# Kernel optimization log

Measured on AMD Instinct MI355X. Metric: run time of the kernel, lower is better.

## Reference

```python
import jax, jax.numpy as jnp
import numpy as np

N = 128  # image size
J = 4    # number of scales
L = 4    # number of orientations


def make_morlet_filters(n, j_max, n_angles):
    """Fixed Morlet filter bank in Fourier space, shape [J, L, N, N] (real)."""
    freqs = np.fft.fftfreq(n) * 2.0 * np.pi
    kx = freqs[:, None] * np.ones((1, n))
    ky = np.ones((n, 1)) * freqs[None, :]
    filters = np.zeros((j_max, n_angles, n, n), dtype=np.float32)
    for j in range(j_max):
        k0 = 3.0 * np.pi / 4.0 / (2.0 ** j)   # central frequency of scale j
        sigma = 0.8 * (2.0 ** j)               # gaussian width in space
        for l in range(n_angles):
            theta = np.pi * l / n_angles
            k0x, k0y = k0 * np.cos(theta), k0 * np.sin(theta)
            beta = np.exp(-0.5 * sigma ** 2 * k0 ** 2)  # zero-mean correction
            g_shift = np.exp(-0.5 * sigma ** 2 * ((kx - k0x) ** 2 + (ky - k0y) ** 2))
            g_zero = np.exp(-0.5 * sigma ** 2 * (kx ** 2 + ky ** 2))
            filters[j, l] = g_shift - beta * g_zero
    return jnp.asarray(filters)


PSI = make_morlet_filters(N, J, L)  # fixed (non-learned) filter bank
VALID_PAIRS = [(j1, j2) for j1 in range(J) for j2 in range(J) if j2 > j1]  # 6 pairs


def setup_inputs() -> dict:
    key = jax.random.key(0)
    k1, k2, k3, k4, k5 = jax.random.split(key, 5)
    B = 64
    return {
        "image_batch": jax.random.normal(k1, (B, N, N), dtype=jnp.float32),
        "fc1_w": jax.random.normal(k2, (4, 11), dtype=jnp.float32) * 0.3,
        "fc1_b": jax.random.normal(k3, (4,), dtype=jnp.float32) * 0.1,
        "fc2_w": jax.random.normal(k4, (10, 4), dtype=jnp.float32) * 0.3,
        "fc2_b": jax.random.normal(k5, (10,), dtype=jnp.float32) * 0.1,
    }


def _scattering(image):
    # image: [B, N, N]
    i_hat = jnp.fft.fft2(image)  # [B,N,N] complex64
    s0 = jnp.mean(image, axis=(1, 2))  # [B]
    # first order: |x * psi_{j1,l1}|  -> [B,J,L,N,N]
    u1 = jnp.abs(jnp.fft.ifft2(i_hat[:, None, None] * PSI[None]))
    s1 = jnp.mean(u1, axis=(2, 3, 4))  # [B,J] averaged over orientations+space
    u1_hat = jnp.fft.fft2(u1)  # [B,J,L,N,N]
    # second order: only j2 > j1 (others NaN in original and masked out)
    s2_list = []
    for (j1, j2) in VALID_PAIRS:
        # [B, L1, L2, N, N]
        field = jnp.fft.ifft2(u1_hat[:, j1, :, None] * PSI[j2][None, None])
        s2_list.append(jnp.mean(jnp.abs(field), axis=(1, 2, 3, 4)))
    s2 = jnp.stack(s2_list, axis=1)  # [B,6]
    return jnp.concatenate([s0[:, None], s1, s2], axis=1)  # [B,11]


def reference(image_batch, fc1_w, fc1_b, fc2_w, fc2_b):
    coeffs = _scattering(image_batch)                      # [B,11]
    h = jax.nn.relu(coeffs @ fc1_w.T + fc1_b)              # [B,4]
    return jax.nn.sigmoid(h @ fc2_w.T + fc2_b)             # [B,10]
```

## Files before the change

kernel.cpp:

```cpp
#include <hip/hip_runtime.h>
#include <math.h>

#define NN   128
#define SS   129
#define TT   512
#define NPIX 16384
#define EPT  32
#define SG   65
#define SG32 33


__device__ __forceinline__ float2 cmul(float2 a, float2 w) {
    return make_float2(a.x * w.x - a.y * w.y, a.x * w.y + a.y * w.x);
}
__device__ __forceinline__ float2 cmulc(float2 a, float2 w) {
    return make_float2(a.x * w.x + a.y * w.y, a.y * w.x - a.x * w.y);
}

template<int SGN>
__device__ __forceinline__ void fft4(float2* f) {
    float2 t0 = make_float2(f[0].x + f[2].x, f[0].y + f[2].y);
    float2 t1 = make_float2(f[0].x - f[2].x, f[0].y - f[2].y);
    float2 t2 = make_float2(f[1].x + f[3].x, f[1].y + f[3].y);
    float2 t3 = make_float2(f[1].x - f[3].x, f[1].y - f[3].y);
// ... 73 lines not shown
    if (tid < 128) {
        float s, c;
        __sincosf((float)tid * 0.04908738521234052f, &s, &c);
        tw[tid] = make_float2(c, s);
    }
}

__device__ __forceinline__ float pass32x4(float4* __restrict__ P4a,
                                          float4* __restrict__ P4b,
                                          const float2* __restrict__ tw, int tid) {
    __syncthreads();
    {
        float4* P = (tid & 256) ? P4b : P4a;
        int line = tid & 31, a = (tid >> 5) & 7;
        float2 f0[4], f1[4];
        #pragma unroll
        for (int kb = 0; kb < 4; ++kb) {
            float4 v = P[(4 * a + kb) * SG32 + line];
            f0[kb] = make_float2(v.x, v.y); f1[kb] = make_float2(v.z, v.w);
        }
        fft4<1>(f0); fft4<1>(f1);
        #pragma unroll
        for (int t = 0; t < 4; ++t) {
            float2 w = tw[4 * t * a];
            float2 aa = cmul(f0[t], w), d = cmul(f1[t], w);
            P[(4 * a + t) * SG32 + line] = make_float4(aa.x, aa.y, d.x, d.y);
        }
    }
    __syncthreads();
    if (tid < 256) {
        float4* P = (tid & 128) ? P4b : P4a;
        int line = tid & 31, t = (tid >> 5) & 3;
        float2 f0[8], f1[8];
        #pragma unroll
        for (int a = 0; a < 8; ++a) {
            float4 v = P[(4 * a + t) * SG32 + line];
            f0[a] = make_float2(v.x, v.y); f1[a] = make_float2(v.z, v.w);
        }
        fft8<1>(f0); fft8<1>(f1);
        #pragma unroll
        for (int n1 = 0; n1 < 8; ++n1)
            P[(4 * n1 + t) * SG32 + line] =
                make_float4(f0[n1].x, f0[n1].y, f1[n1].x, f1[n1].y);
    }
    __syncthreads();
    {
        float4* P = (tid & 256) ? P4b : P4a;
        int row = tid & 31, a = (tid >> 5) & 7;
        float4* R = P + row * SG32 + 4 * a;
        float2 f0[4], f1[4];
        #pragma unroll
        for (int kb = 0; kb < 4; ++kb) {
            float4 v = R[kb];
            f0[kb] = make_float2(v.x, v.y); f1[kb] = make_float2(v.z, v.w);
        }
        fft4<1>(f0); fft4<1>(f1);
        #pragma unroll
        for (int t = 0; t < 4; ++t) {
            float2 w = tw[4 * t * a];
            float2 aa = cmul(f0[t], w), d = cmul(f1[t], w);
            R[t] = make_float4(aa.x, aa.y, d.x, d.y);
        }
    }
    __syncthreads();
    float a2 = 0.f;
    if (tid < 256) {
        float4* P = (tid & 128) ? P4b : P4a;
        int row = tid & 31, t = (tid >> 5) & 3;
        float4* R = P + row * SG32 + t;
        float2 f0[8], f1[8];
        #pragma unroll
        for (int a = 0; a < 8; ++a) {
            float4 v = R[4 * a];
            f0[a] = make_float2(v.x, v.y); f1[a] = make_float2(v.z, v.w);
        }
        fft8<1>(f0); fft8<1>(f1);
        #pragma unroll
        for (int n1 = 0; n1 < 8; ++n1) {
            a2 += sqrtf(f0[n1].x * f0[n1].x + f0[n1].y * f0[n1].y);
            a2 += sqrtf(f1[n1].x * f1[n1].x + f1[n1].y * f1[n1].y);
        }
    }
    return a2;
}

template<int ES, int LS>
__device__ __forceinline__ void fwdA(float2* __restrict__ F,
                                     const float2* __restrict__ tw, int tid) {
    #pragma unroll
    for (int i = 0; i < 4; ++i) {
        int u = i * TT + tid;
        int t = u >> 7, x = u & 127;
        float2* M = F + x * LS;
        float2 f[8];
        #pragma unroll
        for (int n1 = 0; n1 < 8; ++n1) f[n1] = M[(t + 16 * n1) * ES];
        fft8<-1>(f);
        #pragma unroll
        for (int ka = 0; ka < 8; ++ka)
            M[(t + 16 * ka) * ES] = cmulc(f[ka], tw[t * ka]);
    }
}

template<int ES, int LS>
__device__ __forceinline__ void fwdB(float2* __restrict__ F, int tid) {
    #pragma unroll
    for (int i = 0; i < 2; ++i) {
        int u = i * TT + tid;
        int ka = u >> 7, x = u & 127;
        float2* M = F + x * LS;
        float2 g[16];
        #pragma unroll
        for (int t = 0; t < 16; ++t) g[t] = M[(16 * ka + t) * ES];
        fft16<-1>(g);
        #pragma unroll
        for (int kb = 0; kb < 16; ++kb) M[(16 * ka + kb) * ES] = g[kb];
    }
}

__device__ __forceinline__ void fwdB_col_capture(const float2* __restrict__ F, int tid,
                                                 float2* __restrict__ uh) {
    #pragma unroll
    for (int i = 0; i < 2; ++i) {
        int u = i * TT + tid;
        int ka = u >> 7, c = u & 127;
        float2 g[16];
        #pragma unroll
        for (int t = 0; t < 16; ++t) g[t] = F[(16 * ka + t) * SS + c];
        fft16<-1>(g);
        #pragma unroll
        for (int kb = 0; kb < 16; ++kb) uh[i * 16 + kb] = g[kb];
    }
}

template<int ES, int LS>
__device__ __forceinline__ void invA(float2* __restrict__ F,
                                     const float2* __restrict__ tw, int tid) {
    #pragma unroll
    for (int i = 0; i < 2; ++i) {
        int u = i * TT + tid;
        int ka = u >> 7, x = u & 127;
        float2* M = F + x * LS;
        float2 g[16];
        #pragma unroll
        for (int kb = 0; kb < 16; ++kb) g[kb] = M[(16 * ka + kb) * ES];
        fft16<1>(g);
        #pragma unroll
        for (int t = 0; t < 16; ++t)
            M[(16 * ka + t) * ES] = cmul(g[t], tw[t * ka]);
    }
}

template<int ES, int LS>
__device__ __forceinline__ void invB(float2* __restrict__ F, int tid) {
    #pragma unroll
    for (int i = 0; i < 4; ++i) {
        int u = i * TT + tid;
        int t = u >> 7, x = u & 127;
        float2* M = F + x * LS;
        float2 f[8];
        #pragma unroll
        for (int ka = 0; ka < 8; ++ka) f[ka] = M[(16 * ka + t) * ES];
        fft8<1>(f);
        #pragma unroll
        for (int nh = 0; nh < 8; ++nh) M[(t + 16 * nh) * ES] = f[nh];
    }
// ... 25 lines not shown
}

__global__ __attribute__((amdgpu_flat_work_group_size(TT, TT), amdgpu_waves_per_eu(2, 2)))
void k_pre(const float* __restrict__ img,
           float* __restrict__ psi,
           float2* __restrict__ ihat,
           float* __restrict__ coeffs) {
    __shared__ float2 F[NN * SS];
    __shared__ float2 tw[128];
    __shared__ float red[TT / 64];
    int blk = blockIdx.x, tid = threadIdx.x;
    if (blk >= 64) {
        if (blk == 80) {
            for (int i = tid; i < 64 * 11; i += TT)
                if (i % 11 != 0) coeffs[i] = 0.f;
            return;
        }
        int f = blk - 64;
        int j = f >> 2, l = f & 3;
        float k0    = 2.35619449019234493f / (float)(1 << j);
        float sigma = 0.8f * (float)(1 << j);
        float s2    = sigma * sigma;
        float theta = 0.78539816339744831f * (float)l;
        float k0x = k0 * cosf(theta);
        float k0y = k0 * sinf(theta);
        float beta = expf(-0.5f * s2 * k0 * k0);
        const float FSTEP = 0.04908738521234052f;
        float* dst = psi + (size_t)f * NPIX;
        for (int i = tid; i < NPIX; i += TT) {
            int pr = i >> 7, pc = i & 127;
            int kr = (pr >> 4) + 8 * (pr & 15);
            int kc = (pc >> 4) + 8 * (pc & 15);
            float fr = (float)(kr < 64 ? kr : kr - 128) * FSTEP;
            float fc = (float)(kc < 64 ? kc : kc - 128) * FSTEP;
            float dx = fr - k0x, dy = fc - k0y;
            float g1 = expf(-0.5f * s2 * (dx * dx + dy * dy));
            float g0 = expf(-0.5f * s2 * (fr * fr + fc * fc));
            dst[i] = g1 - beta * g0;
        }
        return;
    }
    int b = blk;
    buildTw(tw, tid);
    const float* im = img + (size_t)b * NPIX;
    float acc = 0.f;
    #pragma unroll
    for (int k = 0; k < EPT; ++k) {
        int e = k * TT + tid;
        float v = im[e];
        acc += v;
        F[(e >> 7) * SS + (e & 127)] = make_float2(v, 0.f);
    }
    float ws = waveReduceSum(acc);
    if ((tid & 63) == 0) red[tid >> 6] = ws;
    __syncthreads();
    if (tid == 0) {
        float t = 0.f;
        #pragma unroll
        for (int w = 0; w < TT / 64; ++w) t += red[w];
        coeffs[b * 11 + 0] = t * (1.f / 16384.f);
    }
    fwdA<1, SS>(F, tw, tid);  __syncthreads();
    fwdB<1, SS>(F, tid);      __syncthreads();
    fwdA<SS, 1>(F, tw, tid);  __syncthreads();
    float2 uh[32];
    fwdB_col_capture(F, tid, uh);
    float2* dst = ihat + (size_t)b * NPIX;
    #pragma unroll
    for (int i = 0; i < 2; ++i) {
        int u = i * TT + tid;
        int ka = u >> 7, c = u & 127;
        #pragma unroll
        for (int kb = 0; kb < 16; ++kb)
            dst[(16 * ka + kb) * NN + c] = uh[i * 16 + kb];
    }
}

__global__ __attribute__((amdgpu_flat_work_group_size(TT, TT), amdgpu_waves_per_eu(2, 2)))
void k_scat_big(const float2* __restrict__ ihat,
                const float* __restrict__ psi,
                float* __restrict__ coeffs) {
    __shared__ __align__(16) float2 F[16640];
    __shared__ float2 tw[128];
    float4* G4a = (float4*)F;
    float4* G4b = (float4*)(F + 8320);
    float2* G2a = F;
    float2* G2b = F + 4160;
    float2* G2c = F + 8320;
    float2* G2d = F + 12480;
    float4* P4a = (float4*)F;
    float4* P4b = (float4*)F + 1056;
    int tid = threadIdx.x;
    int x = blockIdx.x;
    int b = x & 63, l1 = x >> 6;
    const float2* ih = ihat + (size_t)b * NPIX;
    const float*  p1 = psi + (size_t)l1 * NPIX;
    buildTw(tw, tid);

    const float S1_128 = 9.3132257461547852e-10f;
    const float S2TR   = 5.6843418860808015e-14f;
    const float S2_03  = 2.2737367544323206e-13f;

    int kalo = tid >> 7, c = tid & 127;
    {
        #pragma unroll
        for (int i = 0; i < 2; ++i) {
            int ka = kalo + 4 * i;
            float2 g[16];
            #pragma unroll
            for (int kb = 0; kb < 16; ++kb) {
                int e = (16 * ka + kb) * NN + c;
                float2 z = ih[e];
                float  p = p1[e];
                g[kb] = make_float2(z.x * p, z.y * p);
            }
            fft16<1>(g);
            #pragma unroll
            for (int t = 0; t < 16; ++t)
                F[(16 * ka + t) * SS + c] = cmul(g[t], tw[t * ka]);
        }
    }
    __syncthreads();
    invB<SS, 1>(F, tid);      __syncthreads();
    invA<1, SS>(F, tw, tid);  __syncthreads();
    float acc = 0.f;
    invBmag_fwdA_row(F, tw, tid, acc);
    float ws1 = waveReduceSum(acc);
    if ((tid & 63) == 0) atomicAdd(&coeffs[b * 11 + 1], ws1 * S1_128);
    __syncthreads();
    fwdB<1, SS>(F, tid);      __syncthreads();
    fwdA<SS, 1>(F, tw, tid);  __syncthreads();
    float2 uh[32];
    fwdB_col_capture(F, tid, uh);
    __syncthreads();

    int m = c & 15;
    bool colKeep = (m < 4) || (m >= 12);
    int pc64 = 8 * (c >> 4) + ((m < 4) ? m : (m - 8));

    {
        const int ORW[4] = {21, 15, 0, -15};
        const int OCW[4] = { 0, 15, 21,  15};
        int fc = (c >> 4) + 8 * (c & 15);
        bool ckw[4]; int pcw[4];
        #pragma unroll
        for (int w = 0; w < 4; ++w) {
            int dc = (fc - OCW[w]) & 127;
            ckw[w] = (dc < 32) || (dc >= 96);
            int uc = (dc < 32) ? dc : (dc - 64);
            pcw[w] = 8 * (uc & 7) + (uc >> 3);
        }
        #pragma unroll
        for (int i = 0; i < 2; ++i) {
            int ka = kalo + 4 * i;
            #pragma unroll
            for (int kb = 0; kb < 16; ++kb) {
                int fr = ka + 8 * kb;
                float2 z = uh[i * 16 + kb];
                int e = (16 * ka + kb) * NN + c;
                #pragma unroll
                for (int w = 0; w < 4; ++w) {
                    if (ckw[w]) {
                        int dr = (fr - ORW[w]) & 127;
                        if (dr < 32 || dr >= 96) {
                            int ur = (dr < 32) ? dr : (dr - 64);
                            int pr = 8 * (ur & 7) + (ur >> 3);
                            float pv = psi[(size_t)(4 + w) * NPIX + e];
                            float2* G = (w == 0) ? G2a : (w == 1) ? G2b
                                       : (w == 2) ? G2c : G2d;
                            G[pr * SG + pcw[w]] = make_float2(z.x * pv, z.y * pv);
                        }
                    }
                }
            }
        }
        __syncthreads();
        {
            int col = tid & 63, k8 = tid >> 6;
            float2 f0[8], f1[8], f2[8], f3[8];
            #pragma unroll
            for (int kb = 0; kb < 8; ++kb) {
                int o = (8 * k8 + kb) * SG + col;
                f0[kb] = G2a[o]; f1[kb] = G2b[o]; f2[kb] = G2c[o]; f3[kb] = G2d[o];
            }
            fft8<1>(f0); fft8<1>(f1); fft8<1>(f2); fft8<1>(f3);
            #pragma unroll
            for (int q = 0; q < 8; ++q) {
                float2 w = tw[2 * q * k8];
                int o = (8 * k8 + q) * SG + col;
                G2a[o] = cmul(f0[q], w); G2b[o] = cmul(f1[q], w);
                G2c[o] = cmul(f2[q], w); G2d[o] = cmul(f3[q], w);
            }
        }
        __syncthreads();
        {
            int col = tid & 63, q = tid >> 6;
            float2 f0[8], f1[8], f2[8], f3[8];
            #pragma unroll
            for (int k8 = 0; k8 < 8; ++k8) {
                int o = (8 * k8 + q) * SG + col;
                f0[k8] = G2a[o]; f1[k8] = G2b[o]; f2[k8] = G2c[o]; f3[k8] = G2d[o];
            }
            fft8<1>(f0); fft8<1>(f1); fft8<1>(f2); fft8<1>(f3);
            #pragma unroll
            for (int n1 = 0; n1 < 8; ++n1) {
                int o = (8 * n1 + q) * SG + col;
                G2a[o] = f0[n1]; G2b[o] = f1[n1]; G2c[o] = f2[n1]; G2d[o] = f3[n1];
            }
        }
        __syncthreads();
        {
            int row = tid & 63, k8 = tid >> 6;
            int base = row * SG + 8 * k8;
            float2 f0[8], f1[8], f2[8], f3[8];
            #pragma unroll
            for (int kb = 0; kb < 8; ++kb) {
                f0[kb] = G2a[base + kb]; f1[kb] = G2b[base + kb];
                f2[kb] = G2c[base + kb]; f3[kb] = G2d[base + kb];
            }
            fft8<1>(f0); fft8<1>(f1); fft8<1>(f2); fft8<1>(f3);
            #pragma unroll
            for (int q = 0; q < 8; ++q) {
                float2 w = tw[2 * q * k8];
                G2a[base + q] = cmul(f0[q], w); G2b[base + q] = cmul(f1[q], w);
                G2c[base + q] = cmul(f2[q], w); G2d[base + q] = cmul(f3[q], w);
            }
        }
        __syncthreads();
        float a2 = 0.f;
        {
            int row = tid & 63, q = tid >> 6;
            int base = row * SG + q;
            float2 f0[8], f1[8], f2[8], f3[8];
            #pragma unroll
            for (int k8 = 0; k8 < 8; ++k8) {
                int o = base + 8 * k8;
                f0[k8] = G2a[o]; f1[k8] = G2b[o]; f2[k8] = G2c[o]; f3[k8] = G2d[o];
            }
            fft8<1>(f0); fft8<1>(f1); fft8<1>(f2); fft8<1>(f3);
            #pragma unroll
            for (int n1 = 0; n1 < 8; ++n1) {
                a2 += sqrtf(f0[n1].x * f0[n1].x + f0[n1].y * f0[n1].y);
                a2 += sqrtf(f1[n1].x * f1[n1].x + f1[n1].y * f1[n1].y);
                a2 += sqrtf(f2[n1].x * f2[n1].x + f2[n1].y * f2[n1].y);
                a2 += sqrtf(f3[n1].x * f3[n1].x + f3[n1].y * f3[n1].y);
            }
        }
        float ws2 = waveReduceSum(a2);
        if ((tid & 63) == 0) atomicAdd(&coeffs[b * 11 + 5 + 0], ws2 * S2TR);
        __syncthreads();
    }

    {
        const float* p0 = psi + (size_t)8 * NPIX;
        const float* pq1 = p0 + NPIX;
        const float* pq2 = pq1 + NPIX;
        const float* pq3 = pq2 + NPIX;
        if (colKeep) {
            #pragma unroll
            for (int i = 0; i < 2; ++i) {
                int ka = kalo + 4 * i;
                #pragma unroll
                for (int kb = 0; kb < 16; ++kb) {
                    if (kb < 4 || kb >= 12) {
                        int pr64 = 8 * ka + ((kb < 4) ? kb : (kb - 8));
                        float2 z = uh[i * 16 + kb];
                        int e = (16 * ka + kb) * NN + c;
                        float a0 = p0[e], a1 = pq1[e], a2f = pq2[e], a3 = pq3[e];
                        G4a[pr64 * SG + pc64] =
                            make_float4(z.x * a0, z.y * a0, z.x * a1, z.y * a1);
                        G4b[pr64 * SG + pc64] =
                            make_float4(z.x * a2f, z.y * a2f, z.x * a3, z.y * a3);
                    }
                }
            }
        }
        __syncthreads();
        {
            int col = tid & 63, k8 = tid >> 6;
            float2 f0[8], f1[8], f2[8], f3[8];
            #pragma unroll
            for (int kb = 0; kb < 8; ++kb) {
                int o = (8 * k8 + kb) * SG + col;
                float4 v = G4a[o];
                f0[kb] = make_float2(v.x, v.y); f1[kb] = make_float2(v.z, v.w);
                float4 u = G4b[o];
                f2[kb] = make_float2(u.x, u.y); f3[kb] = make_float2(u.z, u.w);
            }
            fft8<1>(f0); fft8<1>(f1); fft8<1>(f2); fft8<1>(f3);
            #pragma unroll
            for (int q = 0; q < 8; ++q) {
                float2 w = tw[2 * q * k8];
                int o = (8 * k8 + q) * SG + col;
                float2 a = cmul(f0[q], w), d = cmul(f1[q], w);
                G4a[o] = make_float4(a.x, a.y, d.x, d.y);
                float2 a2c = cmul(f2[q], w), d2 = cmul(f3[q], w);
                G4b[o] = make_float4(a2c.x, a2c.y, d2.x, d2.y);
            }
        }
        __syncthreads();
        {
            int col = tid & 63, q = tid >> 6;
            float2 f0[8], f1[8], f2[8], f3[8];
            #pragma unroll
            for (int k8 = 0; k8 < 8; ++k8) {
                int o = (8 * k8 + q) * SG + col;
                float4 v = G4a[o];
                f0[k8] = make_float2(v.x, v.y); f1[k8] = make_float2(v.z, v.w);
                float4 u = G4b[o];
                f2[k8] = make_float2(u.x, u.y); f3[k8] = make_float2(u.z, u.w);
            }
            fft8<1>(f0); fft8<1>(f1); fft8<1>(f2); fft8<1>(f3);
            #pragma unroll
            for (int n1 = 0; n1 < 8; ++n1) {
                int o = (8 * n1 + q) * SG + col;
                G4a[o] = make_float4(f0[n1].x, f0[n1].y, f1[n1].x, f1[n1].y);
                G4b[o] = make_float4(f2[n1].x, f2[n1].y, f3[n1].x, f3[n1].y);
            }
        }
        __syncthreads();
        {
            int row = tid & 63, k8 = tid >> 6;
            int base = row * SG + 8 * k8;
            float2 f0[8], f1[8], f2[8], f3[8];
            #pragma unroll
            for (int kb = 0; kb < 8; ++kb) {
                float4 v = G4a[base + kb];
                f0[kb] = make_float2(v.x, v.y); f1[kb] = make_float2(v.z, v.w);
                float4 u = G4b[base + kb];
                f2[kb] = make_float2(u.x, u.y); f3[kb] = make_float2(u.z, u.w);
            }
            fft8<1>(f0); fft8<1>(f1); fft8<1>(f2); fft8<1>(f3);
            #pragma unroll
            for (int q = 0; q < 8; ++q) {
                float2 w = tw[2 * q * k8];
                float2 a = cmul(f0[q], w), d = cmul(f1[q], w);
                G4a[base + q] = make_float4(a.x, a.y, d.x, d.y);
                float2 a2c = cmul(f2[q], w), d2 = cmul(f3[q], w);
                G4b[base + q] = make_float4(a2c.x, a2c.y, d2.x, d2.y);
            }
        }
        __syncthreads();
        float a2 = 0.f;
        {
            int row = tid & 63, q = tid >> 6;
            int base = row * SG + q;
            float2 f0[8], f1[8], f2[8], f3[8];
            #pragma unroll
            for (int k8 = 0; k8 < 8; ++k8) {
                float4 v = G4a[base + 8 * k8];
                f0[k8] = make_float2(v.x, v.y); f1[k8] = make_float2(v.z, v.w);
                float4 u = G4b[base + 8 * k8];
                f2[k8] = make_float2(u.x, u.y); f3[k8] = make_float2(u.z, u.w);
            }
            fft8<1>(f0); fft8<1>(f1); fft8<1>(f2); fft8<1>(f3);
            #pragma unroll
            for (int n1 = 0; n1 < 8; ++n1) {
                a2 += sqrtf(f0[n1].x * f0[n1].x + f0[n1].y * f0[n1].y);
                a2 += sqrtf(f1[n1].x * f1[n1].x + f1[n1].y * f1[n1].y);
                a2 += sqrtf(f2[n1].x * f2[n1].x + f2[n1].y * f2[n1].y);
                a2 += sqrtf(f3[n1].x * f3[n1].x + f3[n1].y * f3[n1].y);
            }
        }
        float ws2 = waveReduceSum(a2);
        if ((tid & 63) == 0) atomicAdd(&coeffs[b * 11 + 5 + 1], ws2 * S2TR);
        __syncthreads();
    }

    {
        bool ck32 = (m < 2) || (m >= 14);
        int pc32 = 4 * (c >> 4) + ((m < 2) ? m : (m - 12));
        const float* p0 = psi + (size_t)12 * NPIX;
        const float* pq1 = p0 + NPIX;
        const float* pq2 = pq1 + NPIX;
        const float* pq3 = pq2 + NPIX;
        if (ck32) {
            #pragma unroll
            for (int i = 0; i < 2; ++i) {
                int ka = kalo + 4 * i;
                #pragma unroll
                for (int kb = 0; kb < 16; ++kb) {
                    if (kb < 2 || kb >= 14) {
                        int pr32 = 4 * ka + ((kb < 2) ? kb : (kb - 12));
                        float2 z = uh[i * 16 + kb];
                        int e = (16 * ka + kb) * NN + c;
                        float a0 = p0[e], a1 = pq1[e], a2f = pq2[e], a3 = pq3[e];
                        P4a[pr32 * SG32 + pc32] =
                            make_float4(z.x * a0, z.y * a0, z.x * a1, z.y * a1);
                        P4b[pr32 * SG32 + pc32] =
                            make_float4(z.x * a2f, z.y * a2f, z.x * a3, z.y * a3);
                    }
                }
            }
        }
        float a2 = pass32x4(P4a, P4b, tw, tid);
        float ws2 = waveReduceSum(a2);
        if ((tid & 63) == 0) atomicAdd(&coeffs[b * 11 + 5 + 2], ws2 * S2_03);
    }
}

__global__ __attribute__((amdgpu_flat_work_group_size(TT, TT), amdgpu_waves_per_eu(4, 4)))
void k_scat_small(const float2* __restrict__ ihat,
                  const float* __restrict__ psi,
                  float* __restrict__ coeffs) {
    __shared__ __align__(16) float2 S[8320];
    __shared__ float2 tw[128];
    float2* G2  = S;
    float2* G32 = S;
    float4* G4  = (float4*)S;
    float4* P4a = (float4*)S;
    float4* P4b = (float4*)S + 1056;
    float2* H32 = S + 6144;
    int tid = threadIdx.x;
    int x = blockIdx.x;
    int b = x & 63, l1 = (x >> 6) & 3;
    int t0 = x >> 8;
    int j1 = (t0 == 0) ? 1 : (t0 + 1);
    const float2* ih = ihat + (size_t)b * NPIX;
    const float*  p1 = psi + (size_t)(j1 * 4 + l1) * NPIX;
    buildTw(tw, tid);

    const float S1_64 = 3.7252902984619141e-9f;
    const float S1_32 = 1.4901161193847656e-8f;
    const float S2_32 = 9.0949470177292824e-13f;
    const float S2_V  = 2.2737367544323206e-13f;

    int kalo = tid >> 7, c = tid & 127;

    if (t0 == 0) {
        const int OR1[4] = {21, 15, 0, -15};
        const int OC1[4] = { 0, 15, 21,  15};
        int fc = (c >> 4) + 8 * (c & 15);
        int dc = (fc - OC1[l1]) & 127;
        bool ck = (dc < 32) || (dc >= 96);
        int ucw = (dc < 32) ? dc : (dc - 64);
        int pcd = 8 * (ucw & 7) + (ucw >> 3);
        if (ck) {
            #pragma unroll
            for (int i = 0; i < 2; ++i) {
                int ka = kalo + 4 * i;
                #pragma unroll
                for (int kb = 0; kb < 16; ++kb) {
                    int fr = ka + 8 * kb;
                    int dr = (fr - OR1[l1]) & 127;
                    if (dr < 32 || dr >= 96) {
                        int ur = (dr < 32) ? dr : (dr - 64);
                        int pr = 8 * (ur & 7) + (ur >> 3);
                        int e = (16 * ka + kb) * NN + c;
                        float2 z = ih[e];
                        float  p = p1[e];
                        G2[pr * SG + pcd] = make_float2(z.x * p, z.y * p);
                    }
                }
            }
        }
        __syncthreads();
        {
            int col = tid & 63, k8 = tid >> 6;
            float2 f[8];
            #pragma unroll
            for (int kb = 0; kb < 8; ++kb) f[kb] = G2[(8 * k8 + kb) * SG + col];
            fft8<1>(f);
            #pragma unroll
            for (int q = 0; q < 8; ++q)
                G2[(8 * k8 + q) * SG + col] = cmul(f[q], tw[2 * q * k8]);
        }
        __syncthreads();
        {
            int col = tid & 63, q = tid >> 6;
            float2 f[8];
            #pragma unroll
            for (int k8 = 0; k8 < 8; ++k8) f[k8] = G2[(8 * k8 + q) * SG + col];
            fft8<1>(f);
            #pragma unroll
            for (int n1 = 0; n1 < 8; ++n1) G2[(8 * n1 + q) * SG + col] = f[n1];
        }
        __syncthreads();
        {
            int row = tid & 63, k8 = tid >> 6;
            float2* R = G2 + row * SG + 8 * k8;
            float2 f[8];
            #pragma unroll
            for (int kb = 0; kb < 8; ++kb) f[kb] = R[kb];
            fft8<1>(f);
            #pragma unroll
            for (int q = 0; q < 8; ++q) R[q] = cmul(f[q], tw[2 * q * k8]);
        }
        __syncthreads();
        float acc = 0.f;
        {
            int row = tid & 63, q = tid >> 6;
            float2* R = G2 + row * SG + q;
            float2 f[8];
            #pragma unroll
            for (int k8 = 0; k8 < 8; ++k8) f[k8] = R[8 * k8];
            fft8<1>(f);
            #pragma unroll
            for (int n1 = 0; n1 < 8; ++n1) {
                float mg = sqrtf(f[n1].x * f[n1].x + f[n1].y * f[n1].y);
                acc += mg;
                f[n1] = make_float2(mg, 0.f);
            }
            fft8<-1>(f);
            #pragma unroll
            for (int ka = 0; ka < 8; ++ka)
                R[8 * ka] = cmulc(f[ka], tw[2 * q * ka]);
        }
        float ws1 = waveReduceSum(acc);
        if ((tid & 63) == 0) atomicAdd(&coeffs[b * 11 + 2], ws1 * S1_64);
        __syncthreads();
        {
            int row2 = tid & 63, ka = tid >> 6;
            float2* R2 = G2 + row2 * SG + 8 * ka;
            float2 g[8];
            #pragma unroll
            for (int t = 0; t < 8; ++t) g[t] = R2[t];
            fft8<-1>(g);
            #pragma unroll
            for (int kb = 0; kb < 8; ++kb) R2[kb] = g[kb];
        }
        __syncthreads();
        {
            int col = tid & 63, t = tid >> 6;
            float2 g[8];
            #pragma unroll
            for (int n1 = 0; n1 < 8; ++n1) g[n1] = G2[(t + 8 * n1) * SG + col];
            fft8<-1>(g);
            #pragma unroll
            for (int ka = 0; ka < 8; ++ka)
                G2[(t + 8 * ka) * SG + col] = cmulc(g[ka], tw[2 * t * ka]);
        }
        __syncthreads();
        float2 vh[8];
        int c6 = tid & 63, ka8 = tid >> 6;
        {
            float2 g[8];
            #pragma unroll
            for (int t = 0; t < 8; ++t) g[t] = G2[(8 * ka8 + t) * SG + c6];
            fft8<-1>(g);
            #pragma unroll
            for (int kb = 0; kb < 8; ++kb) vh[kb] = g[kb];
        }
        __syncthreads();

        int uc64 = 8 * (c6 & 7) + (c6 >> 3);
        int fc128 = (uc64 < 32) ? uc64 : (uc64 + 64);
        int scI = 16 * (fc128 & 7) + (fc128 >> 3);
        int se[8];
        #pragma unroll
        for (int kb = 0; kb < 8; ++kb) {
            int ur = 8 * kb + ka8;
            int fr128 = (ur < 32) ? ur : (ur + 64);
            se[kb] = (16 * (fr128 & 7) + (fr128 >> 3)) * NN + scI;
        }

        {
            for (int half = 0; half < 2; ++half) {
                const float* p2a = psi + (size_t)(8 + 2 * half) * NPIX;
                const float* p2b = p2a + NPIX;
                #pragma unroll
                for (int kb = 0; kb < 8; ++kb) {
                    float pa = p2a[se[kb]], pb = p2b[se[kb]];
                    G4[(8 * ka8 + kb) * SG + c6] =
                        make_float4(vh[kb].x * pa, vh[kb].y * pa,
                                    vh[kb].x * pb, vh[kb].y * pb);
                }
                __syncthreads();
                {
                    int col = tid & 63, k8 = tid >> 6;
                    float2 f0[8], f1[8];
                    #pragma unroll
                    for (int kb = 0; kb < 8; ++kb) {
                        float4 v = G4[(8 * k8 + kb) * SG + col];
                        f0[kb] = make_float2(v.x, v.y); f1[kb] = make_float2(v.z, v.w);
                    }
                    fft8<1>(f0); fft8<1>(f1);
                    #pragma unroll
                    for (int q = 0; q < 8; ++q) {
                        float2 w = tw[2 * q * k8];
                        float2 a = cmul(f0[q], w), d = cmul(f1[q], w);
                        G4[(8 * k8 + q) * SG + col] = make_float4(a.x, a.y, d.x, d.y);
                    }
                }
                __syncthreads();
                {
                    int col = tid & 63, q = tid >> 6;
                    float2 f0[8], f1[8];
                    #pragma unroll
                    for (int k8 = 0; k8 < 8; ++k8) {
                        float4 v = G4[(8 * k8 + q) * SG + col];
                        f0[k8] = make_float2(v.x, v.y); f1[k8] = make_float2(v.z, v.w);
                    }
                    fft8<1>(f0); fft8<1>(f1);
                    #pragma unroll
                    for (int n1 = 0; n1 < 8; ++n1)
                        G4[(8 * n1 + q) * SG + col] =
                            make_float4(f0[n1].x, f0[n1].y, f1[n1].x, f1[n1].y);
                }
                __syncthreads();
                {
                    int row = tid & 63, k8 = tid >> 6;
                    float4* R = G4 + row * SG + 8 * k8;
                    float2 f0[8], f1[8];
                    #pragma unroll
                    for (int kb = 0; kb < 8; ++kb) {
                        float4 v = R[kb];
                        f0[kb] = make_float2(v.x, v.y); f1[kb] = make_float2(v.z, v.w);
                    }
                    fft8<1>(f0); fft8<1>(f1);
                    #pragma unroll
                    for (int q = 0; q < 8; ++q) {
                        float2 w = tw[2 * q * k8];
                        float2 a = cmul(f0[q], w), d = cmul(f1[q], w);
                        R[q] = make_float4(a.x, a.y, d.x, d.y);
                    }
                }
                __syncthreads();
                float a2 = 0.f;
                {
                    int row = tid & 63, q = tid >> 6;
                    float4* R = G4 + row * SG + q;
                    float2 f0[8], f1[8];
                    #pragma unroll
                    for (int k8 = 0; k8 < 8; ++k8) {
                        float4 v = R[8 * k8];
                        f0[k8] = make_float2(v.x, v.y); f1[k8] = make_float2(v.z, v.w);
                    }
                    fft8<1>(f0); fft8<1>(f1);
                    #pragma unroll
                    for (int n1 = 0; n1 < 8; ++n1) {
                        a2 += sqrtf(f0[n1].x * f0[n1].x + f0[n1].y * f0[n1].y);
                        a2 += sqrtf(f1[n1].x * f1[n1].x + f1[n1].y * f1[n1].y);
                    }
                }
                float ws2 = waveReduceSum(a2);
                if ((tid & 63) == 0) atomicAdd(&coeffs[b * 11 + 5 + 3], ws2 * S2_V);
                __syncthreads();
            }
        }

        {
            int m6 = c6 & 7;
            bool ckV = (m6 < 2) || (m6 >= 6);
            int p32c = 4 * (c6 >> 3) + ((m6 < 2) ? m6 : (m6 - 4));
            const float* p0 = psi + (size_t)12 * NPIX;
            const float* pq1 = p0 + NPIX;
            const float* pq2 = pq1 + NPIX;
            const float* pq3 = pq2 + NPIX;
            if (ckV) {
                #pragma unroll
                for (int kb = 0; kb < 8; ++kb) {
                    if (kb < 2 || kb >= 6) {
                        int pr32 = 4 * ka8 + (kb & 3);
                        float2 z = vh[kb];
                        float a0 = p0[se[kb]], a1 = pq1[se[kb]];
                        float a2f = pq2[se[kb]], a3 = pq3[se[kb]];
                        P4a[pr32 * SG32 + p32c] =
                            make_float4(z.x * a0, z.y * a0, z.x * a1, z.y * a1);
                        P4b[pr32 * SG32 + p32c] =
                            make_float4(z.x * a2f, z.y * a2f, z.x * a3, z.y * a3);
                    }
                }
            }
            float a2 = pass32x4(P4a, P4b, tw, tid);
            float ws2 = waveReduceSum(a2);
            if ((tid & 63) == 0) atomicAdd(&coeffs[b * 11 + 5 + 4], ws2 * S2_32);
        }
        return;
    }

    if (t0 == 2) {
        int m = c & 15;
        bool ck32 = (m < 2) || (m >= 14);
        int pc32 = 4 * (c >> 4) + ((m < 2) ? m : (m - 12));
        if (ck32) {
            #pragma unroll
            for (int i = 0; i < 2; ++i) {
                int ka = kalo + 4 * i;
                #pragma unroll
                for (int kb = 0; kb < 16; ++kb) {
                    if (kb < 2 || kb >= 14) {
                        int e = (16 * ka + kb) * NN + c;
                        float2 z = ih[e];
                        float  p = p1[e];
                        int pr32 = 4 * ka + ((kb < 2) ? kb : (kb - 12));
                        G32[pr32 * SG32 + pc32] = make_float2(z.x * p, z.y * p);
                    }
                }
            }
        }
        __syncthreads();
        if (tid < 256) {
            int line = tid & 31, a = tid >> 5;
            float2 f[4];
            #pragma unroll
            for (int kb = 0; kb < 4; ++kb) f[kb] = G32[(4 * a + kb) * SG32 + line];
            fft4<1>(f);
            #pragma unroll
            for (int t = 0; t < 4; ++t)
                G32[(4 * a + t) * SG32 + line] = cmul(f[t], tw[4 * t * a]);
        }
        __syncthreads();
        if (tid < 128) {
            int line = tid & 31, t = tid >> 5;
            float2 f[8];
            #pragma unroll
            for (int a = 0; a < 8; ++a) f[a] = G32[(4 * a + t) * SG32 + line];
            fft8<1>(f);
            #pragma unroll
            for (int n1 = 0; n1 < 8; ++n1) G32[(4 * n1 + t) * SG32 + line] = f[n1];
        }
        __syncthreads();
        if (tid < 256) {
            int row = tid & 31, a = tid >> 5;
            float2* R = G32 + row * SG32 + 4 * a;
            float2 f[4];
            #pragma unroll
            for (int kb = 0; kb < 4; ++kb) f[kb] = R[kb];
            fft4<1>(f);
            #pragma unroll
            for (int t = 0; t < 4; ++t) R[t] = cmul(f[t], tw[4 * t * a]);
        }
        __syncthreads();
        float acc = 0.f;
        if (tid < 128) {
            int row = tid & 31, t = tid >> 5;
            float2* R = G32 + row * SG32 + t;
            float2 f[8];
            #pragma unroll
            for (int a = 0; a < 8; ++a) f[a] = R[4 * a];
            fft8<1>(f);
            #pragma unroll
            for (int n1 = 0; n1 < 8; ++n1)
                acc += sqrtf(f[n1].x * f[n1].x + f[n1].y * f[n1].y);
        }
        float ws1 = waveReduceSum(acc);
        if ((tid & 63) == 0 && tid < 128) atomicAdd(&coeffs[b * 11 + 4], ws1 * S1_32);
        return;
    }

    int m = c & 15;
    bool colKeep = (m < 4) || (m >= 12);
    if (colKeep) {
        #pragma unroll
        for (int i = 0; i < 2; ++i) {
            int ka = kalo + 4 * i;
            #pragma unroll
            for (int kb = 0; kb < 16; ++kb) {
                if (kb < 4 || kb >= 12) {
// ... 184 lines not shown
```

Before: 184.5 us.

## Shrink second-order j2=2 paths to per-orientation 32x32 windows and fuse with j2=3

```diff
diff --git a/kernel.cpp b/kernel.cpp
--- a/kernel.cpp
+++ b/kernel.cpp
@@ -179,6 +179,107 @@
         }
     }
     return a2;
+}
+
+__device__ __forceinline__ void pass32combo(float2* __restrict__ Q0, float2* __restrict__ Q1,
+                                            float2* __restrict__ Q2, float2* __restrict__ Q3,
+                                            float4* __restrict__ Pa, float4* __restrict__ Pb,
+                                            const float2* __restrict__ tw, int tid,
+                                            float& aq, float& ap) {
+    __syncthreads();
+    {
+        float2* Qx = (tid & 256) ? Q2 : Q0;
+        float2* Qy = (tid & 256) ? Q3 : Q1;
+        float4* P  = (tid & 256) ? Pb : Pa;
+        int line = tid & 31, a = (tid >> 5) & 7;
+        float2 q0[4], q1[4], f0[4], f1[4];
+        #pragma unroll
+        for (int kb = 0; kb < 4; ++kb) {
+            int o = (4 * a + kb) * SG32 + line;
+            q0[kb] = Qx[o]; q1[kb] = Qy[o];
+            float4 v = P[o];
+            f0[kb] = make_float2(v.x, v.y); f1[kb] = make_float2(v.z, v.w);
+        }
+        fft4<1>(q0); fft4<1>(q1); fft4<1>(f0); fft4<1>(f1);
+        #pragma unroll
+        for (int t = 0; t < 4; ++t) {
+            float2 w = tw[4 * t * a];
+            int o = (4 * a + t) * SG32 + line;
+            Qx[o] = cmul(q0[t], w); Qy[o] = cmul(q1[t], w);
+            float2 aa = cmul(f0[t], w), d = cmul(f1[t], w);
+            P[o] = make_float4(aa.x, aa.y, d.x, d.y);
+        }
+    }
+    __syncthreads();
+    if (tid < 256) {
+        float2* Qx = (tid & 128) ? Q2 : Q0;
+        float2* Qy = (tid & 128) ? Q3 : Q1;
+        float4* P  = (tid & 128) ? Pb : Pa;
+        int line = tid & 31, t = (tid >> 5) & 3;
+        float2 q0[8], q1[8], f0[8], f1[8];
+        #pragma unroll
+        for (int a = 0; a < 8; ++a) {
+            int o = (4 * a + t) * SG32 + line;
+            q0[a] = Qx[o]; q1[a] = Qy[o];
+            float4 v = P[o];
+            f0[a] = make_float2(v.x, v.y); f1[a] = make_float2(v.z, v.w);
+        }
+        fft8<1>(q0); fft8<1>(q1); fft8<1>(f0); fft8<1>(f1);
+        #pragma unroll
+        for (int n1 = 0; n1 < 8; ++n1) {
+            int o = (4 * n1 + t) * SG32 + line;
+            Qx[o] = q0[n1]; Qy[o] = q1[n1];
+            P[o] = make_float4(f0[n1].x, f0[n1].y, f1[n1].x, f1[n1].y);
+        }
+    }
+    __syncthreads();
+    {
+        float2* Qx = (tid & 256) ? Q2 : Q0;
+        float2* Qy = (tid & 256) ? Q3 : Q1;
+        float4* P  = (tid & 256) ? Pb : Pa;
+        int row = tid & 31, a = (tid >> 5) & 7;
+        int base = row * SG32 + 4 * a;
+        float2 q0[4], q1[4], f0[4], f1[4];
+        #pragma unroll
+        for (int kb = 0; kb < 4; ++kb) {
+            q0[kb] = Qx[base + kb]; q1[kb] = Qy[base + kb];
+            float4 v = P[base + kb];
+            f0[kb] = make_float2(v.x, v.y); f1[kb] = make_float2(v.z, v.w);
+        }
+        fft4<1>(q0); fft4<1>(q1); fft4<1>(f0); fft4<1>(f1);
+        #pragma unroll
+        for (int t = 0; t < 4; ++t) {
+            float2 w = tw[4 * t * a];
+            Qx[base + t] = cmul(q0[t], w); Qy[base + t] = cmul(q1[t], w);
+            float2 aa = cmul(f0[t], w), d = cmul(f1[t], w);
+            P[base + t] = make_float4(aa.x, aa.y, d.x, d.y);
+        }
+    }
+    __syncthreads();
+    aq = 0.f; ap = 0.f;
+    if (tid < 256) {
+        float2* Qx = (tid & 128) ? Q2 : Q0;
+        float2* Qy = (tid & 128) ? Q3 : Q1;
+        float4* P  = (tid & 128) ? Pb : Pa;
+        int row = tid & 31, t = (tid >> 5) & 3;
+        int base = row * SG32 + t;
+        float2 q0[8], q1[8], f0[8], f1[8];
+        #pragma unroll
+        for (int a = 0; a < 8; ++a) {
+            int o = base + 4 * a;
+            q0[a] = Qx[o]; q1[a] = Qy[o];
+            float4 v = P[o];
+            f0[a] = make_float2(v.x, v.y); f1[a] = make_float2(v.z, v.w);
+        }
+        fft8<1>(q0); fft8<1>(q1); fft8<1>(f0); fft8<1>(f1);
+        #pragma unroll
+        for (int n1 = 0; n1 < 8; ++n1) {
+            aq += sqrtf(q0[n1].x * q0[n1].x + q0[n1].y * q0[n1].y);
+            aq += sqrtf(q1[n1].x * q1[n1].x + q1[n1].y * q1[n1].y);
+            ap += sqrtf(f0[n1].x * f0[n1].x + f0[n1].y * f0[n1].y);
+            ap += sqrtf(f1[n1].x * f1[n1].x + f1[n1].y * f1[n1].y);
+        }
+    }
 }
 
 template<int ES, int LS>
@@ -370,14 +471,16 @@
                 float* __restrict__ coeffs) {
     __shared__ __align__(16) float2 F[16640];
     __shared__ float2 tw[128];
-    float4* G4a = (float4*)F;
-    float4* G4b = (float4*)(F + 8320);
     float2* G2a = F;
     float2* G2b = F + 4160;
     float2* G2c = F + 8320;
     float2* G2d = F + 12480;
-    float4* P4a = (float4*)F;
-    float4* P4b = (float4*)F + 1056;
+    float2* Q0 = F;
+    float2* Q1 = F + 1056;
+    float2* Q2 = F + 2112;
+    float2* Q3 = F + 3168;
+    float4* Pa = (float4*)(F + 4224);
+    float4* Pb = (float4*)(F + 6336);
     int tid = threadIdx.x;
     int x = blockIdx.x;
     int b = x & 63, l1 = x >> 6;
@@ -423,13 +526,11 @@
     __syncthreads();
 
     int m = c & 15;
-    bool colKeep = (m < 4) || (m >= 12);
-    int pc64 = 8 * (c >> 4) + ((m < 4) ? m : (m - 8));
+    int fc = (c >> 4) + 8 * (c & 15);
 
     {
         const int ORW[4] = {21, 15, 0, -15};
         const int OCW[4] = { 0, 15, 21,  15};
-        int fc = (c >> 4) + 8 * (c & 15);
         bool ckw[4]; int pcw[4];
         #pragma unroll
         for (int w = 0; w < 4; ++w) {
@@ -540,150 +641,60 @@
     }
 
     {
-        const float* p0 = psi + (size_t)8 * NPIX;
-        const float* pq1 = p0 + NPIX;
-        const float* pq2 = pq1 + NPIX;
-        const float* pq3 = pq2 + NPIX;
-        if (colKeep) {
-            #pragma unroll
-            for (int i = 0; i < 2; ++i) {
-                int ka = kalo + 4 * i;
+        const int OR2[4] = {9, 6, 0, -6};
+        const int OC2[4] = {0, 6, 9,  6};
+        bool ckq[4]; int pcq[4];
+        #pragma unroll
+        for (int w = 0; w < 4; ++w) {
+            int dc = (fc - OC2[w]) & 127;
+            ckq[w] = (dc < 16) || (dc >= 112);
+            int f32c = (dc < 16) ? dc : (dc - 96);
+            pcq[w] = 4 * (f32c & 7) + (f32c >> 3);
+        }
+        bool ck32 = (m < 2) || (m >= 14);
+        int pc32 = 4 * (c >> 4) + ((m < 2) ? m : (m - 12));
+        const float* p30 = psi + (size_t)12 * NPIX;
+        #pragma unroll
+        for (int i = 0; i < 2; ++i) {
+            int ka = kalo + 4 * i;
+            #pragma unroll
+            for (int kb = 0; kb < 16; ++kb) {
+                int fr = ka + 8 * kb;
+                float2 z = uh[i * 16 + kb];
+                int e = (16 * ka + kb) * NN + c;
                 #pragma unroll
-                for (int kb = 0; kb < 16; ++kb) {
-                    if (kb < 4 || kb >= 12) {
-                        int pr64 = 8 * ka + ((kb < 4) ? kb : (kb - 8));
-                        float2 z = uh[i * 16 + kb];
-                        int e = (16 * ka + kb) * NN + c;
-                        float a0 = p0[e], a1 = pq1[e], a2f = pq2[e], a3 = pq3[e];
-                        G4a[pr64 * SG + pc64] =
-                            make_float4(z.x * a0, z.y * a0, z.x * a1, z.y * a1);
-                        G4b[pr64 * SG + pc64] =
-                            make_float4(z.x * a2f, z.y * a2f, z.x * a3, z.y * a3);
+                for (int w = 0; w < 4; ++w) {
+                    if (ckq[w]) {
+                        int dr = (fr - OR2[w]) & 127;
+                        if (dr < 16 || dr >= 112) {
+                            int f32r = (dr < 16) ? dr : (dr - 96);
+                            int pr = 4 * (f32r & 7) + (f32r >> 3);
+                            float pv = psi[(size_t)(8 + w) * NPIX + e];
+                            float2* Q = (w == 0) ? Q0 : (w == 1) ? Q1
+                                       : (w == 2) ? Q2 : Q3;
+                            Q[pr * SG32 + pcq[w]] = make_float2(z.x * pv, z.y * pv);
+                        }
                     }
                 }
-            }
-        }
-        __syncthreads();
-        {
-            int col = tid & 63, k8 = tid >> 6;
-            float2 f0[8], f1[8], f2[8], f3[8];
-            #pragma unroll
-            for (int kb = 0; kb < 8; ++kb) {
-                int o = (8 * k8 + kb) * SG + col;
-                float4 v = G4a[o];
-                f0[kb] = make_float2(v.x, v.y); f1[kb] = make_float2(v.z, v.w);
-                float4 u = G4b[o];
-                f2[kb] = make_float2(u.x, u.y); f3[kb] = make_float2(u.z, u.w);
-            }
-            fft8<1>(f0); fft8<1>(f1); fft8<1>(f2); fft8<1>(f3);
-            #pragma unroll
-            for (int q = 0; q < 8; ++q) {
-                float2 w = tw[2 * q * k8];
-                int o = (8 * k8 + q) * SG + col;
-                float2 a = cmul(f0[q], w), d = cmul(f1[q], w);
-                G4a[o] = make_float4(a.x, a.y, d.x, d.y);
-                float2 a2c = cmul(f2[q], w), d2 = cmul(f3[q], w);
-                G4b[o] = make_float4(a2c.x, a2c.y, d2.x, d2.y);
-            }
-        }
-        __syncthreads();
-        {
-            int col = tid & 63, q = tid >> 6;
-            float2 f0[8], f1[8], f2[8], f3[8];
-            #pragma unroll
-            for (int k8 = 0; k8 < 8; ++k8) {
-                int o = (8 * k8 + q) * SG + col;
-                float4 v = G4a[o];
-                f0[k8] = make_float2(v.x, v.y); f1[k8] = make_float2(v.z, v.w);
-                float4 u = G4b[o];
-                f2[k8] = make_float2(u.x, u.y); f3[k8] = make_float2(u.z, u.w);
-            }
-            fft8<1>(f0); fft8<1>(f1); fft8<1>(f2); fft8<1>(f3);
-            #pragma unroll
-            for (int n1 = 0; n1 < 8; ++n1) {
-                int o = (8 * n1 + q) * SG + col;
-                G4a[o] = make_float4(f0[n1].x, f0[n1].y, f1[n1].x, f1[n1].y);
-                G4b[o] = make_float4(f2[n1].x, f2[n1].y, f3[n1].x, f3[n1].y);
-            }
-        }
-        __syncthreads();
-        {
-            int row = tid & 63, k8 = tid >> 6;
-            int base = row * SG + 8 * k8;
-            float2 f0[8], f1[8], f2[8], f3[8];
-            #pragma unroll
-            for (int kb = 0; kb < 8; ++kb) {
-                float4 v = G4a[base + kb];
-                f0[kb] = make_float2(v.x, v.y); f1[kb] = make_float2(v.z, v.w);
-                float4 u = G4b[base + kb];
-                f2[kb] = make_float2(u.x, u.y); f3[kb] = make_float2(u.z, u.w);
-            }
-            fft8<1>(f0); fft8<1>(f1); fft8<1>(f2); fft8<1>(f3);
-            #pragma unroll
-            for (int q = 0; q < 8; ++q) {
-                float2 w = tw[2 * q * k8];
-                float2 a = cmul(f0[q], w), d = cmul(f1[q], w);
-                G4a[base + q] = make_float4(a.x, a.y, d.x, d.y);
-                float2 a2c = cmul(f2[q], w), d2 = cmul(f3[q], w);
-                G4b[base + q] = make_float4(a2c.x, a2c.y, d2.x, d2.y);
-            }
-        }
-        __syncthreads();
-        float a2 = 0.f;
-        {
-            int row = tid & 63, q = tid >> 6;
-            int base = row * SG + q;
-            float2 f0[8], f1[8], f2[8], f3[8];
-            #pragma unroll
-            for (int k8 = 0; k8 < 8; ++k8) {
-                float4 v = G4a[base + 8 * k8];
-                f0[k8] = make_float2(v.x, v.y); f1[k8] = make_float2(v.z, v.w);
-                float4 u = G4b[base + 8 * k8];
-                f2[k8] = make_float2(u.x, u.y); f3[k8] = make_float2(u.z, u.w);
-            }
-            fft8<1>(f0); fft8<1>(f1); fft8<1>(f2); fft8<1>(f3);
-            #pragma unroll
-            for (int n1 = 0; n1 < 8; ++n1) {
-                a2 += sqrtf(f0[n1].x * f0[n1].x + f0[n1].y * f0[n1].y);
-                a2 += sqrtf(f1[n1].x * f1[n1].x + f1[n1].y * f1[n1].y);
-                a2 += sqrtf(f2[n1].x * f2[n1].x + f2[n1].y * f2[n1].y);
-                a2 += sqrtf(f3[n1].x * f3[n1].x + f3[n1].y * f3[n1].y);
-            }
-        }
-        float ws2 = waveReduceSum(a2);
-        if ((tid & 63) == 0) atomicAdd(&coeffs[b * 11 + 5 + 1], ws2 * S2TR);
-        __syncthreads();
-    }
-
-    {
-        bool ck32 = (m < 2) || (m >= 14);
-        int pc32 = 4 * (c >> 4) + ((m < 2) ? m : (m - 12));
-        const float* p0 = psi + (size_t)12 * NPIX;
-        const float* pq1 = p0 + NPIX;
-        const float* pq2 = pq1 + NPIX;
-        const float* pq3 = pq2 + NPIX;
-        if (ck32) {
-            #pragma unroll
-            for (int i = 0; i < 2; ++i) {
-                int ka = kalo + 4 * i;
-                #pragma unroll
-                for (int kb = 0; kb < 16; ++kb) {
-                    if (kb < 2 || kb >= 14) {
-                        int pr32 = 4 * ka + ((kb < 2) ? kb : (kb - 12));
-                        float2 z = uh[i * 16 + kb];
-                        int e = (16 * ka + kb) * NN + c;
-                        float a0 = p0[e], a1 = pq1[e], a2f = pq2[e], a3 = pq3[e];
-                        P4a[pr32 * SG32 + pc32] =
-                            make_float4(z.x * a0, z.y * a0, z.x * a1, z.y * a1);
-                        P4b[pr32 * SG32 + pc32] =
-                            make_float4(z.x * a2f, z.y * a2f, z.x * a3, z.y * a3);
-                    }
+                if (ck32 && (kb < 2 || kb >= 14)) {
+                    int pr32 = 4 * ka + ((kb < 2) ? kb : (kb - 12));
+                    float a0 = p30[e], a1 = p30[NPIX + e];
+                    float a2f = p30[2 * NPIX + e], a3 = p30[3 * NPIX + e];
+                    Pa[pr32 * SG32 + pc32] =
+                        make_float4(z.x * a0, z.y * a0, z.x * a1, z.y * a1);
+                    Pb[pr32 * SG32 + pc32] =
+                        make_float4(z.x * a2f, z.y * a2f, z.x * a3, z.y * a3);
                 }
             }
         }
-        float a2 = pass32x4(P4a, P4b, tw, tid);
-        float ws2 = waveReduceSum(a2);
-        if ((tid & 63) == 0) atomicAdd(&coeffs[b * 11 + 5 + 2], ws2 * S2_03);
+        float aq, ap;
+        pass32combo(Q0, Q1, Q2, Q3, Pa, Pb, tw, tid, aq, ap);
+        float wsq = waveReduceSum(aq);
+        float wsp = waveReduceSum(ap);
+        if ((tid & 63) == 0) {
+            atomicAdd(&coeffs[b * 11 + 5 + 1], wsq * S2_03);
+            atomicAdd(&coeffs[b * 11 + 5 + 2], wsp * S2_03);
+        }
     }
 }
 
@@ -691,13 +702,18 @@
 void k_scat_small(const float2* __restrict__ ihat,
                   const float* __restrict__ psi,
                   float* __restrict__ coeffs) {
-    __shared__ __align__(16) float2 S[8320];
+    __shared__ __align__(16) float2 S[8448];
     __shared__ float2 tw[128];
     float2* G2  = S;
     float2* G32 = S;
-    float4* G4  = (float4*)S;
     float4* P4a = (float4*)S;
     float4* P4b = (float4*)S + 1056;
+    float2* Qs0 = S;
+    float2* Qs1 = S + 1056;
+    float2* Qs2 = S + 2112;
+    float2* Qs3 = S + 3168;
+    float4* Psa = (float4*)(S + 4224);
+    float4* Psb = (float4*)(S + 6336);
     float2* H32 = S + 6144;
     int tid = threadIdx.x;
     int x = blockIdx.x;
@@ -711,7 +727,6 @@
     const float S1_64 = 3.7252902984619141e-9f;
     const float S1_32 = 1.4901161193847656e-8f;
     const float S2_32 = 9.0949470177292824e-13f;
-    const float S2_V  = 2.2737367544323206e-13f;
 
     int kalo = tid >> 7, c = tid & 127;
 
@@ -843,116 +858,57 @@
         }
 
         {
-            for (int half = 0; half < 2; ++half) {
-                const float* p2a = psi + (size_t)(8 + 2 * half) * NPIX;
-                const float* p2b = p2a + NPIX;
-                #pragma unroll
-                for (int kb = 0; kb < 8; ++kb) {
-                    float pa = p2a[se[kb]], pb = p2b[se[kb]];
-                    G4[(8 * ka8 + kb) * SG + c6] =
-                        make_float4(vh[kb].x * pa, vh[kb].y * pa,
-                                    vh[kb].x * pb, vh[kb].y * pb);
-                }
-                __syncthreads();
-                {
-                    int col = tid & 63, k8 = tid >> 6;
-                    float2 f0[8], f1[8];
-                    #pragma unroll
-                    for (int kb = 0; kb < 8; ++kb) {
-                        float4 v = G4[(8 * k8 + kb) * SG + col];
-                        f0[kb] = make_float2(v.x, v.y); f1[kb] = make_float2(v.z, v.w);
-                    }
-                    fft8<1>(f0); fft8<1>(f1);
-                    #pragma unroll
-                    for (int q = 0; q < 8; ++q) {
-                        float2 w = tw[2 * q * k8];
-                        float2 a = cmul(f0[q], w), d = cmul(f1[q], w);
-                        G4[(8 * k8 + q) * SG + col] = make_float4(a.x, a.y, d.x, d.y);
-                    }
-                }
-                __syncthreads();
-                {
-                    int col = tid & 63, q = tid >> 6;
-                    float2 f0[8], f1[8];
-                    #pragma unroll
-                    for (int k8 = 0; k8 < 8; ++k8) {
-                        float4 v = G4[(8 * k8 + q) * SG + col];
-                        f0[k8] = make_float2(v.x, v.y); f1[k8] = make_float2(v.z, v.w);
-                    }
-                    fft8<1>(f0); fft8<1>(f1);
-                    #pragma unroll
-                    for (int n1 = 0; n1 < 8; ++n1)
-                        G4[(8 * n1 + q) * SG + col] =
-                            make_float4(f0[n1].x, f0[n1].y, f1[n1].x, f1[n1].y);
-                }
-                __syncthreads();
-                {
-                    int row = tid & 63, k8 = tid >> 6;
-                    float4* R = G4 + row * SG + 8 * k8;
-                    float2 f0[8], f1[8];
-                    #pragma unroll
-                    for (int kb = 0; kb < 8; ++kb) {
-                        float4 v = R[kb];
-                        f0[kb] = make_float2(v.x, v.y); f1[kb] = make_float2(v.z, v.w);
-                    }
-                    fft8<1>(f0); fft8<1>(f1);
-                    #pragma unroll
-                    for (int q = 0; q < 8; ++q) {
-                        float2 w = tw[2 * q * k8];
-                        float2 a = cmul(f0[q], w), d = cmul(f1[q], w);
-                        R[q] = make_float4(a.x, a.y, d.x, d.y);
-                    }
-                }
-                __syncthreads();
-                float a2 = 0.f;
-                {
-                    int row = tid & 63, q = tid >> 6;
-                    float4* R = G4 + row * SG + q;
-                    float2 f0[8], f1[8];
-                    #pragma unroll
-                    for (int k8 = 0; k8 < 8; ++k8) {
-                        float4 v = R[8 * k8];
-                        f0[k8] = make_float2(v.x, v.y); f1[k8] = make_float2(v.z, v.w);
-                    }
-                    fft8<1>(f0); fft8<1>(f1);
-                    #pragma unroll
-                    for (int n1 = 0; n1 < 8; ++n1) {
-                        a2 += sqrtf(f0[n1].x * f0[n1].x + f0[n1].y * f0[n1].y);
-                        a2 += sqrtf(f1[n1].x * f1[n1].x + f1[n1].y * f1[n1].y);
-                    }
-                }
-                float ws2 = waveReduceSum(a2);
-                if ((tid & 63) == 0) atomicAdd(&coeffs[b * 11 + 5 + 3], ws2 * S2_V);
-                __syncthreads();
-            }
-        }
-
-        {
+            const int OR2[4] = {9, 6, 0, -6};
+            const int OC2[4] = {0, 6, 9,  6};
+            bool ckq[4]; int pcq[4];
+            #pragma unroll
+            for (int w = 0; w < 4; ++w) {
+                int dcw = (uc64 - OC2[w]) & 63;
+                ckq[w] = (dcw < 16) || (dcw >= 48);
+                int f32c = (dcw < 16) ? dcw : (dcw - 32);
+                pcq[w] = 4 * (f32c & 7) + (f32c >> 3);
+            }
             int m6 = c6 & 7;
             bool ckV = (m6 < 2) || (m6 >= 6);
             int p32c = 4 * (c6 >> 3) + ((m6 < 2) ? m6 : (m6 - 4));
-            const float* p0 = psi + (size_t)12 * NPIX;
-            const float* pq1 = p0 + NPIX;
-            const float* pq2 = pq1 + NPIX;
-            const float* pq3 = pq2 + NPIX;
-            if (ckV) {
+            const float* p30 = psi + (size_t)12 * NPIX;
+            #pragma unroll
+            for (int kb = 0; kb < 8; ++kb) {
+                int ur = 8 * kb + ka8;
+                float2 z = vh[kb];
+                int e = se[kb];
                 #pragma unroll
-                for (int kb = 0; kb < 8; ++kb) {
-                    if (kb < 2 || kb >= 6) {
-                        int pr32 = 4 * ka8 + (kb & 3);
-                        float2 z = vh[kb];
-                        float a0 = p0[se[kb]], a1 = pq1[se[kb]];
-                        float a2f = pq2[se[kb]], a3 = pq3[se[kb]];
-                        P4a[pr32 * SG32 + p32c] =
-                            make_float4(z.x * a0, z.y * a0, z.x * a1, z.y * a1);
-                        P4b[pr32 * SG32 + p32c] =
-                            make_float4(z.x * a2f, z.y * a2f, z.x * a3, z.y * a3);
+                for (int w = 0; w < 4; ++w) {
+                    if (ckq[w]) {
+                        int dr = (ur - OR2[w]) & 63;
+                        if (dr < 16 || dr >= 48) {
+                            int f32r = (dr < 16) ? dr : (dr - 32);
+                            int pr = 4 * (f32r & 7) + (f32r >> 3);
+                            float pv = psi[(size_t)(8 + w) * NPIX + e];
+                            float2* Q = (w == 0) ? Qs0 : (w == 1) ? Qs1
+                                       : (w == 2) ? Qs2 : Qs3;
+                            Q[pr * SG32 + pcq[w]] = make_float2(z.x * pv, z.y * pv);
+                        }
                     }
                 }
-            }
-            float a2 = pass32x4(P4a, P4b, tw, tid);
-            float ws2 = waveReduceSum(a2);
-            if ((tid & 63) == 0) atomicAdd(&coeffs[b * 11 + 5 + 4], ws2 * S2_32);
+                if (ckV && (kb < 2 || kb >= 6)) {
+                    int pr32 = 4 * ka8 + (kb & 3);
+                    float a0 = p30[e], a1 = p30[NPIX + e];
+                    float a2f = p30[2 * NPIX + e], a3 = p30[3 * NPIX + e];
+                    Psa[pr32 * SG32 + p32c] =
+                        make_float4(z.x * a0, z.y * a0, z.x * a1, z.y * a1);
+                    Psb[pr32 * SG32 + p32c] =
+                        make_float4(z.x * a2f, z.y * a2f, z.x * a3, z.y * a3);
+                }
+            }
+            float aq, ap;
+            pass32combo(Qs0, Qs1, Qs2, Qs3, Psa, Psb, tw, tid, aq, ap);
+            float wsq = waveReduceSum(aq);
+            float wsp = waveReduceSum(ap);
+            if ((tid & 63) == 0) {
+                atomicAdd(&coeffs[b * 11 + 5 + 3], wsq * S2_32);
+                atomicAdd(&coeffs[b * 11 + 5 + 4], wsp * S2_32);
+            }
         }
         return;
     }
```

Result: no change. 182.6 us (-1.0%).
